# Performance work log

Measured on AMD Instinct MI355X. Metric: run time of the kernel, lower is better.

The kernel has to match this reference:

```python
import jax, jax.numpy as jnp
import numpy as np

HIDDEN = 4096
R = 4
ALPHA = 8
SCALING = ALPHA / R  # 2.0


def setup_inputs() -> dict:
    key = jax.random.key(0)
    k0, k1, k2, k3, k4 = jax.random.split(key, 5)
    B, S = 2, 4096
    x = jax.random.normal(k0, (B, S, HIDDEN), dtype=jnp.float32)
    # LoRA params (A: [r, in], B: [out, r]); use small random values so
    # gradients flow (original inits B to zeros, A kaiming-uniform).
    lora_q_A = jax.random.normal(k1, (R, HIDDEN), dtype=jnp.float32) * (1.0 / np.sqrt(HIDDEN))
    lora_q_B = jax.random.normal(k2, (HIDDEN, R), dtype=jnp.float32) * 0.02
    lora_v_A = jax.random.normal(k3, (R, HIDDEN), dtype=jnp.float32) * (1.0 / np.sqrt(HIDDEN))
    lora_v_B = jax.random.normal(k4, (HIDDEN, R), dtype=jnp.float32) * 0.02
    return {"x": x, "lora_q_A": lora_q_A, "lora_q_B": lora_q_B,
            "lora_v_A": lora_v_A, "lora_v_B": lora_v_B}


def _lora_delta(h, A, B):
    # h: [b, s, d]; A: [r, d]; B: [d, r].  delta = ((h @ A.T) @ B.T) * scaling
    low = jnp.einsum('bsd,rd->bsr', h, A)       # [b, s, r] (r=4, cheap)
    return jnp.einsum('bsr,dr->bsd', low, B) * SCALING


def reference(x, lora_q_A, lora_q_B, lora_v_A, lora_v_B):
    residual = x
    h = x + _lora_delta(x, lora_q_A, lora_q_B)
    h = h + _lora_delta(h, lora_v_A, lora_v_B)
    return h + residual
```

## Files before the change

### kernel.cpp

```cpp
#include <hip/hip_runtime.h>

#define H 4096
#define THREADS 256
#define ROWS 2
#define CHUNKS 4

__device__ __forceinline__ float dot4(float4 a, float4 b) {
    return a.x * b.x + a.y * b.y + a.z * b.z + a.w * b.w;
}

__device__ __forceinline__ unsigned pack_bf16(float a, float b) {
    unsigned ua = __float_as_uint(a), ub = __float_as_uint(b);
    ua = (ua + 0x7FFFu + ((ua >> 16) & 1u)) >> 16;
    ub = (ub + 0x7FFFu + ((ub >> 16) & 1u)) >> 16;
    return ua | (ub << 16);
}
__device__ __forceinline__ float unpack_lo(unsigned p) { return __uint_as_float(p << 16); }
__device__ __forceinline__ float unpack_hi(unsigned p) { return __uint_as_float(p & 0xFFFF0000u); }

__global__ void __launch_bounds__(THREADS) compute_C_kernel(
    const float* __restrict__ A_v, const float* __restrict__ B_q,
    float* __restrict__ C)
{
    const int tid = threadIdx.x;
    float acc[4][4];
#pragma unroll
    for (int i = 0; i < 4; ++i)
#pragma unroll
        for (int j = 0; j < 4; ++j) acc[i][j] = 0.f;

#pragma unroll
    for (int c = 0; c < CHUNKS; ++c) {
        const int d0 = c * (THREADS * 4) + tid * 4;
        float avf[4][4], bqf[4][4];
#pragma unroll
        for (int r = 0; r < 4; ++r) {
            float4 t = *reinterpret_cast<const float4*>(A_v + (size_t)r * H + d0);
            avf[r][0] = t.x; avf[r][1] = t.y; avf[r][2] = t.z; avf[r][3] = t.w;
        }
#pragma unroll
        for (int i = 0; i < 4; ++i) {
            float4 t = *reinterpret_cast<const float4*>(B_q + (size_t)(d0 + i) * 4);
            bqf[i][0] = t.x; bqf[i][1] = t.y; bqf[i][2] = t.z; bqf[i][3] = t.w;
        }
#pragma unroll
        for (int i = 0; i < 4; ++i)
#pragma unroll
            for (int rp = 0; rp < 4; ++rp)
#pragma unroll
                for (int r = 0; r < 4; ++r)
                    acc[rp][r] += avf[rp][i] * bqf[i][r];
    }

    const int lane = tid & 63, wave = tid >> 6;
    __shared__ float red[4][16];
#pragma unroll
    for (int rp = 0; rp < 4; ++rp)
#pragma unroll
        for (int r = 0; r < 4; ++r) {
            float v = acc[rp][r];
#pragma unroll
            for (int off = 32; off; off >>= 1) v += __shfl_down(v, off, 64);
            if (lane == 0) red[wave][rp * 4 + r] = v;
        }
    __syncthreads();
    if (tid < 16) C[tid] = red[0][tid] + red[1][tid] + red[2][tid] + red[3][tid];
}

__global__ void __launch_bounds__(THREADS) lora_fused_kernel(
    const float* __restrict__ x,
    const float* __restrict__ A_q, const float* __restrict__ B_q,
    const float* __restrict__ A_v, const float* __restrict__ B_v,
    const float* __restrict__ C,
    float* __restrict__ out)
{
    const int tid = threadIdx.x;
    const size_t row0 = (size_t)blockIdx.x * ROWS;
    const float* xbase = x + row0 * H;

    unsigned xp[ROWS][CHUNKS][2];
    float accq[ROWS][4], accv[ROWS][4];
#pragma unroll
    for (int m = 0; m < ROWS; ++m)
#pragma unroll
        for (int r = 0; r < 4; ++r) { accq[m][r] = 0.f; accv[m][r] = 0.f; }

#pragma unroll
    for (int c = 0; c < CHUNKS; ++c) {
        const int d0 = c * (THREADS * 4) + tid * 4;
        float4 xv[ROWS];
#pragma unroll
        for (int m = 0; m < ROWS; ++m) {
            xv[m] = *reinterpret_cast<const float4*>(xbase + (size_t)m * H + d0);
            xp[m][c][0] = pack_bf16(xv[m].x, xv[m].y);
            xp[m][c][1] = pack_bf16(xv[m].z, xv[m].w);
        }
#pragma unroll
        for (int r = 0; r < 4; ++r) {
            float4 aq = *reinterpret_cast<const float4*>(A_q + (size_t)r * H + d0);
#pragma unroll
            for (int m = 0; m < ROWS; ++m) accq[m][r] += dot4(xv[m], aq);
        }
#pragma unroll
        for (int r = 0; r < 4; ++r) {
            float4 av = *reinterpret_cast<const float4*>(A_v + (size_t)r * H + d0);
#pragma unroll
            for (int m = 0; m < ROWS; ++m) accv[m][r] += dot4(xv[m], av);
        }
    }

    const int lane = tid & 63, wave = tid >> 6;
    __shared__ float red[4][16];
    __shared__ float sums[16];
#pragma unroll
    for (int i = 0; i < 16; ++i) {
        const int m = i >> 3, v = i & 7;
        float s = (v < 4) ? accq[m][v] : accv[m][v - 4];
#pragma unroll
        for (int off = 1; off < 64; off <<= 1) s += __shfl_xor(s, off, 64);
        if (lane == 0) red[wave][i] = s;
    }
    __syncthreads();
    if (tid < 16) sums[tid] = red[0][tid] + red[1][tid] + red[2][tid] + red[3][tid];
    __syncthreads();

    float lq2[ROWS][4], lv2[ROWS][4];
    {
        float cm[16];
#pragma unroll
        for (int i = 0; i < 16; ++i) cm[i] = C[i];
#pragma unroll
        for (int m = 0; m < ROWS; ++m) {
#pragma unroll
            for (int r = 0; r < 4; ++r) lq2[m][r] = 2.f * sums[m * 8 + r];
#pragma unroll
            for (int rp = 0; rp < 4; ++rp) {
                float s = sums[m * 8 + 4 + rp];
#pragma unroll
                for (int r = 0; r < 4; ++r) s += sums[m * 8 + r] * 2.f * cm[rp * 4 + r];
                lv2[m][rp] = 2.f * s;
            }
        }
    }

#pragma unroll
    for (int c = 0; c < CHUNKS; ++c) {
        const int d0 = c * (THREADS * 4) + tid * 4;
        float o[ROWS][4];
#pragma unroll
        for (int i = 0; i < 4; ++i) {
            float4 bq = *reinterpret_cast<const float4*>(B_q + (size_t)(d0 + i) * 4);
            float4 bv = *reinterpret_cast<const float4*>(B_v + (size_t)(d0 + i) * 4);
#pragma unroll
            for (int m = 0; m < ROWS; ++m) {
                const unsigned p = xp[m][c][i >> 1];
                const float xs = (i & 1) ? unpack_hi(p) : unpack_lo(p);
                float dq = lq2[m][0] * bq.x + lq2[m][1] * bq.y + lq2[m][2] * bq.z + lq2[m][3] * bq.w;
                float dv = lv2[m][0] * bv.x + lv2[m][1] * bv.y + lv2[m][2] * bv.z + lv2[m][3] * bv.w;
                o[m][i] = 2.f * xs + dq + dv;
            }
        }
#pragma unroll
        for (int m = 0; m < ROWS; ++m) {
            float4 ov = make_float4(o[m][0], o[m][1], o[m][2], o[m][3]);
            *reinterpret_cast<float4*>(out + (row0 + m) * H + d0) = ov;
        }
    }
}

extern "C" void kernel_launch(void* const* d_in, const int* in_sizes, int n_in,
                              void* d_out, int out_size, void* d_ws, size_t ws_size,
                              hipStream_t stream) {
    const float* x   = (const float*)d_in[0];
    const float* A_q = (const float*)d_in[1];
    const float* B_q = (const float*)d_in[2];
    const float* A_v = (const float*)d_in[3];
    const float* B_v = (const float*)d_in[4];
    float* out = (float*)d_out;
    float* C   = (float*)d_ws;

    const int nrows = in_sizes[0] / H;

    compute_C_kernel<<<1, THREADS, 0, stream>>>(A_v, B_q, C);
    lora_fused_kernel<<<nrows / ROWS, THREADS, 0, stream>>>(
        x, A_q, B_q, A_v, B_v, C, out);
}
```

Baseline: 94.10 us.

## Pre-pack LoRA weights to interleaved bf16 and stage x in LDS

A prep kernel now also converts A_q/A_v and B_q/B_v into interleaved bf16 packs, so each thread loads one contiguous 64-byte group per column chunk instead of eight strided float4 loads. The main kernel keeps the bf16 copy of x in shared memory rather than registers and disables unrolling of the chunk loops, which lowers register pressure. This is meant to cut weight-load traffic and raise occupancy, at the cost of bf16 rounding of the weights and extra LDS use.

```diff
diff --git a/kernel.cpp b/kernel.cpp
--- a/kernel.cpp
+++ b/kernel.cpp
@@ -4,10 +4,7 @@
 #define THREADS 256
 #define ROWS 2
 #define CHUNKS 4
-
-__device__ __forceinline__ float dot4(float4 a, float4 b) {
-    return a.x * b.x + a.y * b.y + a.z * b.z + a.w * b.w;
-}
+#define NCLUMP (H / 4)
 
 __device__ __forceinline__ unsigned pack_bf16(float a, float b) {
     unsigned ua = __float_as_uint(a), ub = __float_as_uint(b);
@@ -18,59 +15,108 @@
 __device__ __forceinline__ float unpack_lo(unsigned p) { return __uint_as_float(p << 16); }
 __device__ __forceinline__ float unpack_hi(unsigned p) { return __uint_as_float(p & 0xFFFF0000u); }
 
-__global__ void __launch_bounds__(THREADS) compute_C_kernel(
-    const float* __restrict__ A_v, const float* __restrict__ B_q,
-    float* __restrict__ C)
+__global__ void __launch_bounds__(THREADS) prep_kernel(
+    const float* __restrict__ A_q, const float* __restrict__ B_q,
+    const float* __restrict__ A_v, const float* __restrict__ B_v,
+    float* __restrict__ C, uint4* __restrict__ Apk, uint4* __restrict__ Bpk)
 {
     const int tid = threadIdx.x;
-    float acc[4][4];
-#pragma unroll
-    for (int i = 0; i < 4; ++i)
-#pragma unroll
-        for (int j = 0; j < 4; ++j) acc[i][j] = 0.f;
-
-#pragma unroll
-    for (int c = 0; c < CHUNKS; ++c) {
-        const int d0 = c * (THREADS * 4) + tid * 4;
-        float avf[4][4], bqf[4][4];
-#pragma unroll
-        for (int r = 0; r < 4; ++r) {
-            float4 t = *reinterpret_cast<const float4*>(A_v + (size_t)r * H + d0);
-            avf[r][0] = t.x; avf[r][1] = t.y; avf[r][2] = t.z; avf[r][3] = t.w;
-        }
-#pragma unroll
-        for (int i = 0; i < 4; ++i) {
-            float4 t = *reinterpret_cast<const float4*>(B_q + (size_t)(d0 + i) * 4);
-            bqf[i][0] = t.x; bqf[i][1] = t.y; bqf[i][2] = t.z; bqf[i][3] = t.w;
-        }
+    if (blockIdx.x == 0) {
+        float acc[4][4];
 #pragma unroll
         for (int i = 0; i < 4; ++i)
 #pragma unroll
-            for (int rp = 0; rp < 4; ++rp)
-#pragma unroll
-                for (int r = 0; r < 4; ++r)
-                    acc[rp][r] += avf[rp][i] * bqf[i][r];
-    }
-
-    const int lane = tid & 63, wave = tid >> 6;
-    __shared__ float red[4][16];
-#pragma unroll
-    for (int rp = 0; rp < 4; ++rp)
-#pragma unroll
-        for (int r = 0; r < 4; ++r) {
-            float v = acc[rp][r];
-#pragma unroll
-            for (int off = 32; off; off >>= 1) v += __shfl_down(v, off, 64);
-            if (lane == 0) red[wave][rp * 4 + r] = v;
-        }
-    __syncthreads();
-    if (tid < 16) C[tid] = red[0][tid] + red[1][tid] + red[2][tid] + red[3][tid];
-}
+            for (int j = 0; j < 4; ++j) acc[i][j] = 0.f;
+#pragma unroll
+        for (int c = 0; c < CHUNKS; ++c) {
+            const int d0 = c * (THREADS * 4) + tid * 4;
+            float avf[4][4], bqf[4][4];
+#pragma unroll
+            for (int r = 0; r < 4; ++r) {
+                float4 t = *reinterpret_cast<const float4*>(A_v + (size_t)r * H + d0);
+                avf[r][0] = t.x; avf[r][1] = t.y; avf[r][2] = t.z; avf[r][3] = t.w;
+            }
+#pragma unroll
+            for (int i = 0; i < 4; ++i) {
+                float4 t = *reinterpret_cast<const float4*>(B_q + (size_t)(d0 + i) * 4);
+                bqf[i][0] = t.x; bqf[i][1] = t.y; bqf[i][2] = t.z; bqf[i][3] = t.w;
+            }
+#pragma unroll
+            for (int i = 0; i < 4; ++i)
+#pragma unroll
+                for (int rp = 0; rp < 4; ++rp)
+#pragma unroll
+                    for (int r = 0; r < 4; ++r)
+                        acc[rp][r] += avf[rp][i] * bqf[i][r];
+        }
+        const int lane = tid & 63, wave = tid >> 6;
+        __shared__ float red[4][16];
+#pragma unroll
+        for (int rp = 0; rp < 4; ++rp)
+#pragma unroll
+            for (int r = 0; r < 4; ++r) {
+                float v = acc[rp][r];
+#pragma unroll
+                for (int off = 32; off; off >>= 1) v += __shfl_down(v, off, 64);
+                if (lane == 0) red[wave][rp * 4 + r] = v;
+            }
+        __syncthreads();
+        if (tid < 16) C[tid] = red[0][tid] + red[1][tid] + red[2][tid] + red[3][tid];
+        return;
+    }
+
+    const int g = (int)(blockIdx.x - 1) * THREADS + tid;
+    if (g < NCLUMP) {
+        const int d0 = g * 4;
+        uint4 w[4];
+#pragma unroll
+        for (int j = 0; j < 2; ++j) {
+            const float* src = j ? A_v : A_q;
+#pragma unroll
+            for (int p = 0; p < 2; ++p) {
+                float4 r0 = *reinterpret_cast<const float4*>(src + (size_t)(2 * p) * H + d0);
+                float4 r1 = *reinterpret_cast<const float4*>(src + (size_t)(2 * p + 1) * H + d0);
+                w[j * 2 + p] = make_uint4(pack_bf16(r0.x, r0.y), pack_bf16(r0.z, r0.w),
+                                          pack_bf16(r1.x, r1.y), pack_bf16(r1.z, r1.w));
+            }
+        }
+#pragma unroll
+        for (int j = 0; j < 4; ++j) Apk[g * 4 + j] = w[j];
+    } else if (g < 2 * NCLUMP) {
+        const int i = g - NCLUMP;
+        const int d0 = i * 4;
+        uint4 w[4];
+#pragma unroll
+        for (int j = 0; j < 2; ++j) {
+            const float* src = j ? B_v : B_q;
+#pragma unroll
+            for (int p = 0; p < 2; ++p) {
+                float4 e0 = *reinterpret_cast<const float4*>(src + (size_t)(d0 + 2 * p) * 4);
+                float4 e1 = *reinterpret_cast<const float4*>(src + (size_t)(d0 + 2 * p + 1) * 4);
+                w[j * 2 + p] = make_uint4(pack_bf16(e0.x, e0.y), pack_bf16(e0.z, e0.w),
+                                          pack_bf16(e1.x, e1.y), pack_bf16(e1.z, e1.w));
+            }
+        }
+#pragma unroll
+        for (int j = 0; j < 4; ++j) Bpk[i * 4 + j] = w[j];
+    }
+}
+
+#define ACC_PAIR(q, acc, rb)                                                  \
+    {                                                                         \
+        float f0 = unpack_lo((q).x), f1 = unpack_hi((q).x);                   \
+        float f2 = unpack_lo((q).y), f3 = unpack_hi((q).y);                   \
+        acc[0][rb] += xv0.x * f0 + xv0.y * f1 + xv0.z * f2 + xv0.w * f3;      \
+        acc[1][rb] += xv1.x * f0 + xv1.y * f1 + xv1.z * f2 + xv1.w * f3;      \
+        f0 = unpack_lo((q).z); f1 = unpack_hi((q).z);                         \
+        f2 = unpack_lo((q).w); f3 = unpack_hi((q).w);                         \
+        acc[0][rb + 1] += xv0.x * f0 + xv0.y * f1 + xv0.z * f2 + xv0.w * f3;  \
+        acc[1][rb + 1] += xv1.x * f0 + xv1.y * f1 + xv1.z * f2 + xv1.w * f3;  \
+    }
 
 __global__ void __launch_bounds__(THREADS) lora_fused_kernel(
     const float* __restrict__ x,
-    const float* __restrict__ A_q, const float* __restrict__ B_q,
-    const float* __restrict__ A_v, const float* __restrict__ B_v,
+    const uint4* __restrict__ Apk, const uint4* __restrict__ Bpk,
     const float* __restrict__ C,
     float* __restrict__ out)
 {
@@ -78,40 +124,32 @@
     const size_t row0 = (size_t)blockIdx.x * ROWS;
     const float* xbase = x + row0 * H;
 
-    unsigned xp[ROWS][CHUNKS][2];
-    float accq[ROWS][4], accv[ROWS][4];
-#pragma unroll
-    for (int m = 0; m < ROWS; ++m)
-#pragma unroll
-        for (int r = 0; r < 4; ++r) { accq[m][r] = 0.f; accv[m][r] = 0.f; }
-
-#pragma unroll
-    for (int c = 0; c < CHUNKS; ++c) {
-        const int d0 = c * (THREADS * 4) + tid * 4;
-        float4 xv[ROWS];
-#pragma unroll
-        for (int m = 0; m < ROWS; ++m) {
-            xv[m] = *reinterpret_cast<const float4*>(xbase + (size_t)m * H + d0);
-            xp[m][c][0] = pack_bf16(xv[m].x, xv[m].y);
-            xp[m][c][1] = pack_bf16(xv[m].z, xv[m].w);
-        }
-#pragma unroll
-        for (int r = 0; r < 4; ++r) {
-            float4 aq = *reinterpret_cast<const float4*>(A_q + (size_t)r * H + d0);
-#pragma unroll
-            for (int m = 0; m < ROWS; ++m) accq[m][r] += dot4(xv[m], aq);
-        }
-#pragma unroll
-        for (int r = 0; r < 4; ++r) {
-            float4 av = *reinterpret_cast<const float4*>(A_v + (size_t)r * H + d0);
-#pragma unroll
-            for (int m = 0; m < ROWS; ++m) accv[m][r] += dot4(xv[m], av);
-        }
-    }
-
-    const int lane = tid & 63, wave = tid >> 6;
+    __shared__ uint2 xlds[ROWS][NCLUMP];
     __shared__ float red[4][16];
     __shared__ float sums[16];
+
+    float accq[ROWS][4], accv[ROWS][4];
+#pragma unroll
+    for (int m = 0; m < ROWS; ++m)
+#pragma unroll
+        for (int r = 0; r < 4; ++r) { accq[m][r] = 0.f; accv[m][r] = 0.f; }
+
+#pragma unroll 1
+    for (int c = 0; c < CHUNKS; ++c) {
+        const int idx = c * THREADS + tid;
+        const float4 xv0 = *reinterpret_cast<const float4*>(xbase + (size_t)idx * 4);
+        const float4 xv1 = *reinterpret_cast<const float4*>(xbase + H + (size_t)idx * 4);
+        xlds[0][idx] = make_uint2(pack_bf16(xv0.x, xv0.y), pack_bf16(xv0.z, xv0.w));
+        xlds[1][idx] = make_uint2(pack_bf16(xv1.x, xv1.y), pack_bf16(xv1.z, xv1.w));
+        const uint4* ap = Apk + (size_t)idx * 4;
+        const uint4 a0 = ap[0], a1 = ap[1], a2 = ap[2], a3 = ap[3];
+        ACC_PAIR(a0, accq, 0)
+        ACC_PAIR(a1, accq, 2)
+        ACC_PAIR(a2, accv, 0)
+        ACC_PAIR(a3, accv, 2)
+    }
+
+    const int lane = tid & 63, wave = tid >> 6;
 #pragma unroll
     for (int i = 0; i < 16; ++i) {
         const int m = i >> 3, v = i & 7;
@@ -143,28 +181,34 @@
         }
     }
 
-#pragma unroll
+#pragma unroll 1
     for (int c = 0; c < CHUNKS; ++c) {
-        const int d0 = c * (THREADS * 4) + tid * 4;
-        float o[ROWS][4];
-#pragma unroll
-        for (int i = 0; i < 4; ++i) {
-            float4 bq = *reinterpret_cast<const float4*>(B_q + (size_t)(d0 + i) * 4);
-            float4 bv = *reinterpret_cast<const float4*>(B_v + (size_t)(d0 + i) * 4);
-#pragma unroll
-            for (int m = 0; m < ROWS; ++m) {
-                const unsigned p = xp[m][c][i >> 1];
-                const float xs = (i & 1) ? unpack_hi(p) : unpack_lo(p);
-                float dq = lq2[m][0] * bq.x + lq2[m][1] * bq.y + lq2[m][2] * bq.z + lq2[m][3] * bq.w;
-                float dv = lv2[m][0] * bv.x + lv2[m][1] * bv.y + lv2[m][2] * bv.z + lv2[m][3] * bv.w;
-                o[m][i] = 2.f * xs + dq + dv;
-            }
-        }
-#pragma unroll
-        for (int m = 0; m < ROWS; ++m) {
-            float4 ov = make_float4(o[m][0], o[m][1], o[m][2], o[m][3]);
-            *reinterpret_cast<float4*>(out + (row0 + m) * H + d0) = ov;
-        }
+        const int idx = c * THREADS + tid;
+        const uint4* bp = Bpk + (size_t)idx * 4;
+        const uint4 b0 = bp[0], b1 = bp[1], b2 = bp[2], b3 = bp[3];
+        const uint2 xp0 = xlds[0][idx], xp1 = xlds[1][idx];
+        float o0[4], o1[4];
+#pragma unroll
+        for (int k = 0; k < 4; ++k) {
+            const unsigned wq0 = (k == 0) ? b0.x : (k == 1) ? b0.z : (k == 2) ? b1.x : b1.z;
+            const unsigned wq1 = (k == 0) ? b0.y : (k == 1) ? b0.w : (k == 2) ? b1.y : b1.w;
+            const unsigned wv0 = (k == 0) ? b2.x : (k == 1) ? b2.z : (k == 2) ? b3.x : b3.z;
+            const unsigned wv1 = (k == 0) ? b2.y : (k == 1) ? b2.w : (k == 2) ? b3.y : b3.w;
+            const unsigned xw0 = (k < 2) ? xp0.x : xp0.y;
+            const unsigned xw1 = (k < 2) ? xp1.x : xp1.y;
+            const float xs0 = (k & 1) ? unpack_hi(xw0) : unpack_lo(xw0);
+            const float xs1 = (k & 1) ? unpack_hi(xw1) : unpack_lo(xw1);
+            const float q0 = unpack_lo(wq0), q1 = unpack_hi(wq0), q2 = unpack_lo(wq1), q3 = unpack_hi(wq1);
+            const float v0 = unpack_lo(wv0), v1 = unpack_hi(wv0), v2 = unpack_lo(wv1), v3 = unpack_hi(wv1);
+            o0[k] = 2.f * xs0 + lq2[0][0] * q0 + lq2[0][1] * q1 + lq2[0][2] * q2 + lq2[0][3] * q3
+                              + lv2[0][0] * v0 + lv2[0][1] * v1 + lv2[0][2] * v2 + lv2[0][3] * v3;
+            o1[k] = 2.f * xs1 + lq2[1][0] * q0 + lq2[1][1] * q1 + lq2[1][2] * q2 + lq2[1][3] * q3
+                              + lv2[1][0] * v0 + lv2[1][1] * v1 + lv2[1][2] * v2 + lv2[1][3] * v3;
+        }
+        *reinterpret_cast<float4*>(out + row0 * H + (size_t)idx * 4) =
+            make_float4(o0[0], o0[1], o0[2], o0[3]);
+        *reinterpret_cast<float4*>(out + (row0 + 1) * H + (size_t)idx * 4) =
+            make_float4(o1[0], o1[1], o1[2], o1[3]);
     }
 }
 
@@ -177,11 +221,13 @@
     const float* A_v = (const float*)d_in[3];
     const float* B_v = (const float*)d_in[4];
     float* out = (float*)d_out;
+
     float* C   = (float*)d_ws;
+    uint4* Apk = (uint4*)((char*)d_ws + 256);
+    uint4* Bpk = (uint4*)((char*)d_ws + 256 + 64 * 1024);
 
     const int nrows = in_sizes[0] / H;
 
-    compute_C_kernel<<<1, THREADS, 0, stream>>>(A_v, B_q, C);
-    lora_fused_kernel<<<nrows / ROWS, THREADS, 0, stream>>>(
-        x, A_q, B_q, A_v, B_v, C, out);
-}
+    prep_kernel<<<9, THREADS, 0, stream>>>(A_q, B_q, A_v, B_v, C, Apk, Bpk);
+    lora_fused_kernel<<<nrows / ROWS, THREADS, 0, stream>>>(x, Apk, Bpk, C, out);
+}
```

After: 96.13 us. +2.2%, slower.
